# Optimization experiments

Measured on AMD Instinct MI355X. Metric: run time of the kernel, lower is better.

Reference implementation:

```python
import jax, jax.numpy as jnp
import numpy as np

TILE = 128

def _dequant(Wq, scales, zeros):
    # Wq: [out, n_cols] int codes; scales/zeros: [n_tiles, out]
    n_cols = Wq.shape[1]
    tids = jnp.arange(n_cols) // TILE            # tile id per column
    s = scales[tids].T                           # [out, n_cols]
    z = zeros[tids].T                            # [out, n_cols]
    return (Wq.astype(jnp.float32) - z) * s

def setup_inputs() -> dict:
    key = jax.random.key(0)
    ks = jax.random.split(key, 9)
    B, IN, OUT = 256, 8192, 8192
    n_high, n_low = 2048, 6144
    nt_hi, nt_lo = 16, 48
    x = jax.random.normal(ks[0], (B, IN), dtype=jnp.float32)
    W_high_q = jax.random.randint(ks[1], (OUT, n_high), 0, 64, dtype=jnp.int32)
    W_low_q = jax.random.randint(ks[2], (OUT, n_low), 0, 32, dtype=jnp.int32)
    scales_high = jax.random.uniform(ks[3], (nt_hi, OUT), dtype=jnp.float32, minval=0.001, maxval=0.05)
    zeros_high = jax.random.normal(ks[4], (nt_hi, OUT), dtype=jnp.float32) * 16.0
    scales_low = jax.random.uniform(ks[5], (nt_lo, OUT), dtype=jnp.float32, minval=0.001, maxval=0.05)
    zeros_low = jax.random.normal(ks[6], (nt_lo, OUT), dtype=jnp.float32) * 8.0
    bias = jax.random.normal(ks[7], (OUT,), dtype=jnp.float32) * 0.02
    col_indices = jax.random.permutation(ks[8], IN).astype(jnp.int32)
    return {"x": x, "W_high_q": W_high_q, "W_low_q": W_low_q,
            "scales_high": scales_high, "zeros_high": zeros_high,
            "scales_low": scales_low, "zeros_low": zeros_low,
            "bias": bias, "col_indices": col_indices}

def reference(x, W_high_q, W_low_q, scales_high, zeros_high,
              scales_low, zeros_low, bias, col_indices):
    # Dequantize both precision regions (per-tile affine: (q - zero) * scale)
    W_high = _dequant(W_high_q, scales_high, zeros_high)   # [out, n_high]
    W_low = _dequant(W_low_q, scales_low, zeros_low)       # [out, n_low]
    W_perm = jnp.concatenate([W_high, W_low], axis=1)      # [out, in]
    # y = x @ W.T where W[:, col_indices] = W_perm  <=>  gather x columns instead
    x_perm = x[:, col_indices]                             # [B, in]
    return x_perm @ W_perm.T + bias[None, :]
```

## Files before the change

### kernel.cpp

```cpp
#include <hip/hip_runtime.h>
#include <stdint.h>


#define IN_DIM 8192
#define OUT_DIM 8192
#define BDIM 256
#define NH 2048
#define NL 6144
#define BN 64
#define BK 32
#define KSPLIT 4
#define KSEG (IN_DIM / KSPLIT)
#define NSTEP (KSEG / BK)

typedef __bf16 bf16x8 __attribute__((ext_vector_type(8)));
typedef float f32x4 __attribute__((ext_vector_type(4)));

__device__ __forceinline__ unsigned short bfbits(float f) {
  union { float f; unsigned int u; } v; v.f = f;
  unsigned int u = v.u;
  u += 0x7fffu + ((u >> 16) & 1u);
  return (unsigned short)(u >> 16);
}
__device__ __forceinline__ unsigned int pk2(float a, float b) {
  return (unsigned int)bfbits(a) | ((unsigned int)bfbits(b) << 16);
}

extern "C" __global__ void gather_k(const float* __restrict__ x,
                                    const int* __restrict__ ci,
                                    unsigned short* __restrict__ xp) {
  int i4 = blockIdx.x * blockDim.x + threadIdx.x;
  int b = i4 >> 11;
  int k4 = (i4 & 2047) << 2;
  int4 c = *(const int4*)(ci + k4);
  const float* xr = x + (size_t)b * IN_DIM;
  uint2 st;
  st.x = pk2(xr[c.x], xr[c.y]);
  st.y = pk2(xr[c.z], xr[c.w]);
  *(uint2*)(xp + (size_t)b * IN_DIM + k4) = st;
}

extern "C" __global__ __launch_bounds__(256, 2)
void gemm_k(const unsigned short* __restrict__ xp,
            const int* __restrict__ Whq, const int* __restrict__ Wlq,
            const float* __restrict__ sh, const float* __restrict__ zh,
            const float* __restrict__ sl, const float* __restrict__ zl,
            const float* __restrict__ bias,
            float* __restrict__ outp,
            int use_atomic)
{
  __shared__ char smem[2 * 16384 + 2 * 4096];
  const int t = threadIdx.x;
  const int lane = t & 63;
  const int wv = t >> 6;
  const int nblk = blockIdx.x;
  const int kh = blockIdx.y;
  const int n0 = nblk * BN;
  const int l15 = lane & 15;
  const int g4 = lane >> 4;

  const int xr = t >> 2;
  const int xc = (t & 3) ^ (xr & 3);
  const unsigned short* xg0 = xp + (size_t)xr * IN_DIM + (size_t)kh * KSEG + xc * 8;

  const int wcol = t >> 2;
  const int wm = t & 3;
  const int oo = n0 + wcol;
  const int* wb0 = (kh == 0) ? (Whq + (size_t)oo * NH)
                             : (Wlq + (size_t)oo * NL + (size_t)(kh - 1) * KSEG);
  const float* sb = (kh == 0) ? (sh + oo) : (sl + (size_t)(kh - 1) * 16 * OUT_DIM + oo);
  const float* zb = (kh == 0) ? (zh + oo) : (zl + (size_t)(kh - 1) * 16 * OUT_DIM + oo);

  f32x4 acc[4][4];
  {
    float bvj[4];
    #pragma unroll
    for (int j = 0; j < 4; ++j)
      bvj[j] = (kh == 0) ? bias[n0 + j * 16 + l15] : 0.f;
    #pragma unroll
    for (int i = 0; i < 4; ++i)
      #pragma unroll
      for (int j = 0; j < 4; ++j) {
        acc[i][j][0] = bvj[j]; acc[i][j][1] = bvj[j];
        acc[i][j][2] = bvj[j]; acc[i][j][3] = bvj[j];
      }
  }

  int4 q0, q1; float sc, zs;

  auto stage_x = [&](int bx, int s) {
    const unsigned short* g = xg0 + s * BK;
    char* lb = smem + bx * 16384 + wv * 1024;
    #pragma unroll
    for (int r = 0; r < 4; ++r)
      __builtin_amdgcn_global_load_lds(
          (const __attribute__((address_space(1))) void*)(g + (size_t)r * 64 * IN_DIM),
          (__attribute__((address_space(3))) void*)(lb + r * 4096), 16, 0, 0);
  };
  auto stage_w_load = [&](int s) {
    const int* p = wb0 + s * BK + wm * 8;
    q0 = *(const int4*)p;
    q1 = *(const int4*)(p + 4);
    float s_ = sb[(s >> 2) * OUT_DIM];
    float z_ = zb[(s >> 2) * OUT_DIM];
    sc = s_; zs = z_ * s_;
  };
  auto stage_w_write = [&](int bx) {
    uint4 d;
    d.x = pk2((float)q0.x * sc - zs, (float)q0.y * sc - zs);
    d.y = pk2((float)q0.z * sc - zs, (float)q0.w * sc - zs);
    d.z = pk2((float)q1.x * sc - zs, (float)q1.y * sc - zs);
    d.w = pk2((float)q1.z * sc - zs, (float)q1.w * sc - zs);
    char* wb = smem + 32768 + bx * 4096;
    *(uint4*)(wb + wcol * 64 + ((wm ^ (wcol & 3)) * 16)) = d;
  };
  auto compute = [&](int bx) {
    const char* xb = smem + bx * 16384;
    const char* wbuf = smem + 32768 + bx * 4096;
    bf16x8 a[4], b[4];
    #pragma unroll
    for (int i = 0; i < 4; ++i) {
      int row = wv * 64 + i * 16 + l15;
      int ch = g4 ^ (row & 3);
      a[i] = *(const bf16x8*)(xb + row * 64 + ch * 16);
    }
    #pragma unroll
    for (int j = 0; j < 4; ++j) {
      int col = j * 16 + l15;
      int ch = g4 ^ (col & 3);
      b[j] = *(const bf16x8*)(wbuf + col * 64 + ch * 16);
    }
    #pragma unroll
    for (int i = 0; i < 4; ++i)
      #pragma unroll
      for (int j = 0; j < 4; ++j)
        acc[i][j] = __builtin_amdgcn_mfma_f32_16x16x32_bf16(a[i], b[j], acc[i][j], 0, 0, 0);
  };

  stage_x(0, 0);
  stage_w_load(0);
  stage_w_write(0);
  __syncthreads();

  #pragma unroll 1
  for (int s = 0; s < NSTEP; s += 2) {
    stage_x(1, s + 1);
    stage_w_load(s + 1);
    compute(0);
    stage_w_write(1);
    __syncthreads();
    if (s + 2 < NSTEP) { stage_x(0, s + 2); stage_w_load(s + 2); }
    compute(1);
    if (s + 2 < NSTEP) stage_w_write(0);
    __syncthreads();
  }

  if (use_atomic) {
    #pragma unroll
    for (int i = 0; i < 4; ++i) {
      int row0 = wv * 64 + i * 16 + g4 * 4;
      #pragma unroll
      for (int j = 0; j < 4; ++j) {
        int col = n0 + j * 16 + l15;
        #pragma unroll
        for (int r = 0; r < 4; ++r)
          atomicAdd(&outp[(size_t)(row0 + r) * OUT_DIM + col], acc[i][j][r]);
      }
    }
  } else {
    float* pp = outp + (size_t)kh * ((size_t)BDIM * OUT_DIM);
    #pragma unroll
    for (int i = 0; i < 4; ++i) {
      int row0 = wv * 64 + i * 16 + g4 * 4;
      #pragma unroll
      for (int j = 0; j < 4; ++j) {
        int col = n0 + j * 16 + l15;
        #pragma unroll
        for (int r = 0; r < 4; ++r)
          pp[(size_t)(row0 + r) * OUT_DIM + col] = acc[i][j][r];
      }
    }
  }
}

extern "C" __global__ void reduce_k(const float* __restrict__ part,
                                    float* __restrict__ out) {
  int i4 = blockIdx.x * blockDim.x + threadIdx.x;
  size_t off = (size_t)i4 * 4;
  const size_t S = (size_t)BDIM * OUT_DIM;
  float4 p0 = *(const float4*)(part + off);
  float4 p1 = *(const float4*)(part + off + S);
  float4 p2 = *(const float4*)(part + off + 2 * S);
  float4 p3 = *(const float4*)(part + off + 3 * S);
  float4 r;
  r.x = p0.x + p1.x + p2.x + p3.x;
  r.y = p0.y + p1.y + p2.y + p3.y;
  r.z = p0.z + p1.z + p2.z + p3.z;
  r.w = p0.w + p1.w + p2.w + p3.w;
  *(float4*)(out + off) = r;
}

extern "C" void kernel_launch(void* const* d_in, const int* in_sizes, int n_in,
                              void* d_out, int out_size, void* d_ws, size_t ws_size,
                              hipStream_t stream) {
  const float* x   = (const float*)d_in[0];
  const int* Whq   = (const int*)d_in[1];
  const int* Wlq   = (const int*)d_in[2];
  const float* sh  = (const float*)d_in[3];
  const float* zh  = (const float*)d_in[4];
  const float* sl  = (const float*)d_in[5];
  const float* zl  = (const float*)d_in[6];
  const float* bias = (const float*)d_in[7];
  const int* ci    = (const int*)d_in[8];
  float* out = (float*)d_out;

  unsigned short* xp = (unsigned short*)d_ws;
  const size_t XP_BYTES = (size_t)BDIM * IN_DIM * 2;
  const size_t PART_BYTES = (size_t)KSPLIT * BDIM * OUT_DIM * 4;
  bool have_ws = ws_size >= XP_BYTES + PART_BYTES;

  gather_k<<<dim3(2048), dim3(256), 0, stream>>>(x, ci, xp);

  dim3 gg(OUT_DIM / BN, KSPLIT);
  if (have_ws) {
    float* part = (float*)((char*)d_ws + XP_BYTES);
    gemm_k<<<gg, dim3(256), 0, stream>>>(xp, Whq, Wlq, sh, zh, sl, zl, bias, part, 0);
    reduce_k<<<dim3(2048), dim3(256), 0, stream>>>(part, out);
  } else {
    hipMemsetAsync(d_out, 0, (size_t)out_size * sizeof(float), stream);
    gemm_k<<<gg, dim3(256), 0, stream>>>(xp, Whq, Wlq, sh, zh, sl, zl, bias, out, 1);
  }
}
```

Measured before the change: 398.6 us.

## Prefetch quantized weights two steps ahead and stage scales in LDS

Preloads all per-tile scales and scale*zero products for the block into shared memory once, instead of fetching them from global memory each step. Weight codes are now loaded two K-steps ahead into double register sets, so global latency has more compute to hide behind. The loop is peeled and uses hand-placed waitcnt, s_barrier and sched_barrier in place of __syncthreads, which allows partial vmcnt waits. This raises register pressure and makes correctness depend on the exact waitcnt counts.

```diff
diff --git a/kernel.cpp b/kernel.cpp
--- a/kernel.cpp
+++ b/kernel.cpp
@@ -12,6 +12,12 @@
 #define KSPLIT 4
 #define KSEG (IN_DIM / KSPLIT)
 #define NSTEP (KSEG / BK)
+#define NTILE (KSEG / 128)
+
+#define XOFF 0
+#define WOFF 32768
+#define SCOFF 40960
+#define ZSOFF 45056
 
 typedef __bf16 bf16x8 __attribute__((ext_vector_type(8)));
 typedef float f32x4 __attribute__((ext_vector_type(4)));
@@ -49,13 +55,12 @@
             float* __restrict__ outp,
             int use_atomic)
 {
-  __shared__ char smem[2 * 16384 + 2 * 4096];
+  __shared__ char smem[49152];
   const int t = threadIdx.x;
   const int lane = t & 63;
   const int wv = t >> 6;
-  const int nblk = blockIdx.x;
   const int kh = blockIdx.y;
-  const int n0 = nblk * BN;
+  const int n0 = blockIdx.x * BN;
   const int l15 = lane & 15;
   const int g4 = lane >> 4;
 
@@ -65,11 +70,10 @@
 
   const int wcol = t >> 2;
   const int wm = t & 3;
-  const int oo = n0 + wcol;
-  const int* wb0 = (kh == 0) ? (Whq + (size_t)oo * NH)
-                             : (Wlq + (size_t)oo * NL + (size_t)(kh - 1) * KSEG);
-  const float* sb = (kh == 0) ? (sh + oo) : (sl + (size_t)(kh - 1) * 16 * OUT_DIM + oo);
-  const float* zb = (kh == 0) ? (zh + oo) : (zl + (size_t)(kh - 1) * 16 * OUT_DIM + oo);
+  const int* wb0 = (kh == 0) ? (Whq + (size_t)(n0 + wcol) * NH)
+                             : (Wlq + (size_t)(n0 + wcol) * NL + (size_t)(kh - 1) * KSEG);
+  const float* sbase = ((kh == 0) ? sh : sl + (size_t)(kh - 1) * NTILE * OUT_DIM) + n0;
+  const float* zbase = ((kh == 0) ? zh : zl + (size_t)(kh - 1) * NTILE * OUT_DIM) + n0;
 
   f32x4 acc[4][4];
   {
@@ -86,37 +90,34 @@
       }
   }
 
-  int4 q0, q1; float sc, zs;
-
   auto stage_x = [&](int bx, int s) {
     const unsigned short* g = xg0 + s * BK;
-    char* lb = smem + bx * 16384 + wv * 1024;
+    char* lb = smem + XOFF + bx * 16384 + wv * 1024;
     #pragma unroll
     for (int r = 0; r < 4; ++r)
       __builtin_amdgcn_global_load_lds(
           (const __attribute__((address_space(1))) void*)(g + (size_t)r * 64 * IN_DIM),
           (__attribute__((address_space(3))) void*)(lb + r * 4096), 16, 0, 0);
   };
-  auto stage_w_load = [&](int s) {
+  auto wload = [&](int4& a, int4& b, int s) {
     const int* p = wb0 + s * BK + wm * 8;
-    q0 = *(const int4*)p;
-    q1 = *(const int4*)(p + 4);
-    float s_ = sb[(s >> 2) * OUT_DIM];
-    float z_ = zb[(s >> 2) * OUT_DIM];
-    sc = s_; zs = z_ * s_;
-  };
-  auto stage_w_write = [&](int bx) {
+    a = *(const int4*)p;
+    b = *(const int4*)(p + 4);
+  };
+  auto wdeq = [&](int bx, int4 a, int4 b, int s) {
+    int tl = s >> 2;
+    float sc = *(const float*)(smem + SCOFF + (tl * 64 + wcol) * 4);
+    float zs = *(const float*)(smem + ZSOFF + (tl * 64 + wcol) * 4);
     uint4 d;
-    d.x = pk2((float)q0.x * sc - zs, (float)q0.y * sc - zs);
-    d.y = pk2((float)q0.z * sc - zs, (float)q0.w * sc - zs);
-    d.z = pk2((float)q1.x * sc - zs, (float)q1.y * sc - zs);
-    d.w = pk2((float)q1.z * sc - zs, (float)q1.w * sc - zs);
-    char* wb = smem + 32768 + bx * 4096;
-    *(uint4*)(wb + wcol * 64 + ((wm ^ (wcol & 3)) * 16)) = d;
+    d.x = pk2((float)a.x * sc - zs, (float)a.y * sc - zs);
+    d.y = pk2((float)a.z * sc - zs, (float)a.w * sc - zs);
+    d.z = pk2((float)b.x * sc - zs, (float)b.y * sc - zs);
+    d.w = pk2((float)b.z * sc - zs, (float)b.w * sc - zs);
+    *(uint4*)(smem + WOFF + bx * 4096 + wcol * 64 + ((wm ^ (wcol & 3)) * 16)) = d;
   };
   auto compute = [&](int bx) {
-    const char* xb = smem + bx * 16384;
-    const char* wbuf = smem + 32768 + bx * 4096;
+    const char* xb = smem + XOFF + bx * 16384;
+    const char* wbuf = smem + WOFF + bx * 4096;
     bf16x8 a[4], b[4];
     #pragma unroll
     for (int i = 0; i < 4; ++i) {
@@ -137,23 +138,53 @@
         acc[i][j] = __builtin_amdgcn_mfma_f32_16x16x32_bf16(a[i], b[j], acc[i][j], 0, 0, 0);
   };
 
+  #pragma unroll
+  for (int r = 0; r < 4; ++r) {
+    int p = t + r * 256;
+    float s_ = sbase[(size_t)(p >> 6) * OUT_DIM + (p & 63)];
+    float z_ = zbase[(size_t)(p >> 6) * OUT_DIM + (p & 63)];
+    *(float*)(smem + SCOFF + p * 4) = s_;
+    *(float*)(smem + ZSOFF + p * 4) = z_ * s_;
+  }
   stage_x(0, 0);
-  stage_w_load(0);
-  stage_w_write(0);
+  int4 qa0, qa1, qb0, qb1;
+  wload(qa0, qa1, 0);
+  wload(qb0, qb1, 1);
   __syncthreads();
+  wdeq(0, qa0, qa1, 0);
+  asm volatile("s_waitcnt lgkmcnt(0)" ::: "memory");
+  __builtin_amdgcn_s_barrier();
 
   #pragma unroll 1
-  for (int s = 0; s < NSTEP; s += 2) {
+  for (int it = 0; it < 31; ++it) {
+    const int s = it * 2;
+    __builtin_amdgcn_sched_barrier(0);
     stage_x(1, s + 1);
-    stage_w_load(s + 1);
+    __builtin_amdgcn_sched_barrier(0);
+    wload(qa0, qa1, s + 2);
+    __builtin_amdgcn_sched_barrier(0);
     compute(0);
-    stage_w_write(1);
-    __syncthreads();
-    if (s + 2 < NSTEP) { stage_x(0, s + 2); stage_w_load(s + 2); }
+    wdeq(1, qb0, qb1, s + 1);
+    asm volatile("s_waitcnt vmcnt(2) lgkmcnt(0)" ::: "memory");
+    __builtin_amdgcn_s_barrier();
+    __builtin_amdgcn_sched_barrier(0);
+    stage_x(0, s + 2);
+    __builtin_amdgcn_sched_barrier(0);
+    wload(qb0, qb1, s + 3);
+    __builtin_amdgcn_sched_barrier(0);
     compute(1);
-    if (s + 2 < NSTEP) stage_w_write(0);
-    __syncthreads();
-  }
+    wdeq(0, qa0, qa1, s + 2);
+    asm volatile("s_waitcnt vmcnt(2) lgkmcnt(0)" ::: "memory");
+    __builtin_amdgcn_s_barrier();
+  }
+  __builtin_amdgcn_sched_barrier(0);
+  stage_x(1, 63);
+  __builtin_amdgcn_sched_barrier(0);
+  compute(0);
+  wdeq(1, qb0, qb1, 63);
+  asm volatile("s_waitcnt vmcnt(0) lgkmcnt(0)" ::: "memory");
+  __builtin_amdgcn_s_barrier();
+  compute(1);
 
   if (use_atomic) {
     #pragma unroll
```

Measured after the change: 388.1 us. -2.6%, faster.

## Widen GEMM tiles, stream int weights to LDS, dequantize in registers

Applied to the files above, without the earlier changes.

Each block now owns 256 output columns over a 1024-wide K segment, with 512 threads and an 8-way K split that maps onto a single 1-D grid. This cuts redundant re-reads of the activation tile across column blocks. Raw int32 weight codes are copied straight into a triple-buffered LDS area with global_load_lds, and per-tile scales and zero·scale products are preloaded into LDS. Dequantization to bf16 happens in registers right before each MFMA, and sched_barrier, setprio and manual vmcnt waits interleave loads with compute. In exchange it uses a large LDS footprint (one block per CU) and writes a larger partial-sum buffer, which the templated reduce kernel then has to read back.

```diff
diff --git a/kernel.cpp b/kernel.cpp
--- a/kernel.cpp
+++ b/kernel.cpp
@@ -7,11 +7,17 @@
 #define BDIM 256
 #define NH 2048
 #define NL 6144
-#define BN 64
+#define BN 256
 #define BK 32
-#define KSPLIT 4
-#define KSEG (IN_DIM / KSPLIT)
-#define NSTEP (KSEG / BK)
+#define KSPLIT 8
+#define KSEG 1024
+#define NTIL 32
+#define NT 8
+
+#define XOFF 0
+#define WOFF 32768
+#define SCOFF 131072
+#define ZSOFF 139264
 
 typedef __bf16 bf16x8 __attribute__((ext_vector_type(8)));
 typedef float f32x4 __attribute__((ext_vector_type(4)));
@@ -26,9 +32,9 @@
   return (unsigned int)bfbits(a) | ((unsigned int)bfbits(b) << 16);
 }
 
-extern "C" __global__ void gather_k(const float* __restrict__ x,
-                                    const int* __restrict__ ci,
-                                    unsigned short* __restrict__ xp) {
+__global__ void gather_k(const float* __restrict__ x,
+                         const int* __restrict__ ci,
+                         unsigned short* __restrict__ xp) {
   int i4 = blockIdx.x * blockDim.x + threadIdx.x;
   int b = i4 >> 11;
   int k4 = (i4 & 2047) << 2;
@@ -40,7 +46,96 @@
   *(uint2*)(xp + (size_t)b * IN_DIM + k4) = st;
 }
 
-extern "C" __global__ __launch_bounds__(256, 2)
+#define PH_OPEN \
+  __builtin_amdgcn_sched_barrier(0); \
+  __builtin_amdgcn_s_barrier(); \
+  __builtin_amdgcn_sched_barrier(0)
+
+#define STAGE_X(S) { \
+  _Pragma("unroll") \
+  for (int q_ = 0; q_ < 2; ++q_) \
+    __builtin_amdgcn_global_load_lds( \
+      (const __attribute__((address_space(1))) void*)(xsrc + (size_t)q_ * 128 * IN_DIM * 2 + (S) * 64), \
+      (__attribute__((address_space(3))) void*)(smem + XOFF + ((S) & 1) * 16384 + q_ * 8192 + wv * 1024), \
+      16, 0, 0); \
+}
+
+#define STAGE_WQ(S, BUF, Q) \
+  __builtin_amdgcn_global_load_lds( \
+    (const __attribute__((address_space(1))) void*)(wsrc + (size_t)(Q) * 64 * ldw + (S) * 32), \
+    (__attribute__((address_space(3))) void*)(smem + WOFF + (BUF) * 32768 + (Q) * 8192 + wv * 1024), \
+    16, 0, 0);
+
+#define BREAD(WBP, J, U0, U1) { \
+  int col_ = wc64 + (J) * 16 + l15; \
+  const char* bp_ = (WBP) + col_ * 128; \
+  U0 = *(const int4*)(bp_ + (((2 * g4) ^ (col_ & 7)) * 16)); \
+  U1 = *(const int4*)(bp_ + (((2 * g4 + 1) ^ (col_ & 7)) * 16)); \
+}
+
+#define MFMA8(BJ, J) { \
+  _Pragma("unroll") \
+  for (int i_ = 0; i_ < 8; ++i_) \
+    acc[i_][J] = __builtin_amdgcn_mfma_f32_16x16x32_bf16(aF[i_], BJ, acc[i_][J], 0, 0, 0); \
+}
+
+#define TILE(T, ISSX, ISSW, VMST) { \
+  const int xb_ = (T) & 1, wb_ = (T) % 3, wb2_ = ((T) + 2) % 3; \
+  const char* xbp_ = smem + XOFF + xb_ * 16384; \
+  const char* wbp_ = smem + WOFF + wb_ * 32768; \
+  const int tl_ = (T) >> 2; \
+   \
+  bf16x8 aF[8]; \
+  _Pragma("unroll") \
+  for (int i_ = 0; i_ < 8; ++i_) { \
+    int row_ = wr128 + i_ * 16 + l15; \
+    aF[i_] = *(const bf16x8*)(xbp_ + row_ * 64 + ((g4 ^ (row_ & 3)) * 16)); \
+  } \
+  float scf_[4], zsf_[4]; \
+  _Pragma("unroll") \
+  for (int j_ = 0; j_ < 4; ++j_) { \
+    int sidx_ = (tl_ * 256 + wc64 + j_ * 16 + l15) * 4; \
+    scf_[j_] = *(const float*)(smem + SCOFF + sidx_); \
+    zsf_[j_] = *(const float*)(smem + ZSOFF + sidx_); \
+  } \
+  int4 u0_, u1_; \
+  BREAD(wbp_, 0, u0_, u1_); \
+  if (ISSX) STAGE_X((T) + 1); \
+  PH_OPEN; \
+  __builtin_amdgcn_s_setprio(1); \
+  { bf16x8 b_ = dq8(u0_, u1_, scf_[0], zsf_[0]); MFMA8(b_, 0); } \
+  __builtin_amdgcn_s_setprio(0); \
+  PH_OPEN; \
+   \
+  BREAD(wbp_, 1, u0_, u1_); \
+  if (ISSW) { STAGE_WQ((T) + 2, wb2_, 0); STAGE_WQ((T) + 2, wb2_, 1); } \
+  PH_OPEN; \
+  __builtin_amdgcn_s_setprio(1); \
+  { bf16x8 b_ = dq8(u0_, u1_, scf_[1], zsf_[1]); MFMA8(b_, 1); } \
+  __builtin_amdgcn_s_setprio(0); \
+  PH_OPEN; \
+   \
+  BREAD(wbp_, 2, u0_, u1_); \
+  if (ISSW) { STAGE_WQ((T) + 2, wb2_, 2); STAGE_WQ((T) + 2, wb2_, 3); } \
+  PH_OPEN; \
+  __builtin_amdgcn_s_setprio(1); \
+  { bf16x8 b_ = dq8(u0_, u1_, scf_[2], zsf_[2]); MFMA8(b_, 2); } \
+  __builtin_amdgcn_s_setprio(0); \
+  PH_OPEN; \
+   \
+  BREAD(wbp_, 3, u0_, u1_); \
+  PH_OPEN; \
+  __builtin_amdgcn_s_setprio(1); \
+  { bf16x8 b_ = dq8(u0_, u1_, scf_[3], zsf_[3]); MFMA8(b_, 3); } \
+  __builtin_amdgcn_s_setprio(0); \
+  __builtin_amdgcn_sched_barrier(0); \
+  VMST; \
+  __builtin_amdgcn_sched_barrier(0); \
+  __builtin_amdgcn_s_barrier(); \
+  __builtin_amdgcn_sched_barrier(0); \
+}
+
+__global__ __launch_bounds__(512, 1)
 void gemm_k(const unsigned short* __restrict__ xp,
             const int* __restrict__ Whq, const int* __restrict__ Wlq,
             const float* __restrict__ sh, const float* __restrict__ zh,
@@ -49,119 +144,81 @@
             float* __restrict__ outp,
             int use_atomic)
 {
-  __shared__ char smem[2 * 16384 + 2 * 4096];
+  __shared__ __attribute__((aligned(16))) char smem[147456];
   const int t = threadIdx.x;
   const int lane = t & 63;
   const int wv = t >> 6;
-  const int nblk = blockIdx.x;
-  const int kh = blockIdx.y;
-  const int n0 = nblk * BN;
+  const int wr128 = (wv >> 2) * 128;
+  const int wc64 = (wv & 3) * 64;
   const int l15 = lane & 15;
   const int g4 = lane >> 4;
 
-  const int xr = t >> 2;
-  const int xc = (t & 3) ^ (xr & 3);
-  const unsigned short* xg0 = xp + (size_t)xr * IN_DIM + (size_t)kh * KSEG + xc * 8;
-
-  const int wcol = t >> 2;
-  const int wm = t & 3;
-  const int oo = n0 + wcol;
-  const int* wb0 = (kh == 0) ? (Whq + (size_t)oo * NH)
-                             : (Wlq + (size_t)oo * NL + (size_t)(kh - 1) * KSEG);
-  const float* sb = (kh == 0) ? (sh + oo) : (sl + (size_t)(kh - 1) * 16 * OUT_DIM + oo);
-  const float* zb = (kh == 0) ? (zh + oo) : (zl + (size_t)(kh - 1) * 16 * OUT_DIM + oo);
-
-  f32x4 acc[4][4];
-  {
-    float bvj[4];
+  const int kh = blockIdx.x & 7;
+  const int n0 = (blockIdx.x >> 3) * BN;
+  const bool hi = (kh < 2);
+
+  const char* xsrc = (const char*)xp + (size_t)(t >> 2) * (IN_DIM * 2)
+                   + (size_t)kh * KSEG * 2 + (((t & 3) ^ ((t >> 2) & 3)) * 16);
+  const int wcol0 = t >> 3;
+  const int ldw = hi ? NH : NL;
+  const int* wsrc = (hi ? Whq + (size_t)kh * KSEG : Wlq + (size_t)(kh - 2) * KSEG)
+                  + (size_t)(n0 + wcol0) * ldw + ((t & 7) ^ (wcol0 & 7)) * 4;
+
+  const float* sbase = (hi ? sh + (size_t)kh * NT * OUT_DIM
+                           : sl + (size_t)(kh - 2) * NT * OUT_DIM) + n0;
+  const float* zbase = (hi ? zh + (size_t)kh * NT * OUT_DIM
+                           : zl + (size_t)(kh - 2) * NT * OUT_DIM) + n0;
+
+  auto dq8 = [&](int4 a, int4 b, float sc, float zs) -> bf16x8 {
+    bf16x8 r;
+    r[0] = (__bf16)((float)a.x * sc - zs);
+    r[1] = (__bf16)((float)a.y * sc - zs);
+    r[2] = (__bf16)((float)a.z * sc - zs);
+    r[3] = (__bf16)((float)a.w * sc - zs);
+    r[4] = (__bf16)((float)b.x * sc - zs);
+    r[5] = (__bf16)((float)b.y * sc - zs);
+    r[6] = (__bf16)((float)b.z * sc - zs);
+    r[7] = (__bf16)((float)b.w * sc - zs);
+    return r;
+  };
+
+  f32x4 acc[8][4];
+  #pragma unroll
+  for (int j = 0; j < 4; ++j) {
+    float bv = (kh == 0) ? bias[n0 + wc64 + j * 16 + l15] : 0.f;
     #pragma unroll
-    for (int j = 0; j < 4; ++j)
-      bvj[j] = (kh == 0) ? bias[n0 + j * 16 + l15] : 0.f;
+    for (int i = 0; i < 8; ++i) {
+      acc[i][j][0] = bv; acc[i][j][1] = bv; acc[i][j][2] = bv; acc[i][j][3] = bv;
+    }
+  }
+
+  #pragma unroll
+  for (int r = 0; r < 4; ++r) {
+    int p = t + r * 512;
+    float s_ = sbase[(size_t)(p >> 8) * OUT_DIM + (p & 255)];
+    float z_ = zbase[(size_t)(p >> 8) * OUT_DIM + (p & 255)];
+    *(float*)(smem + SCOFF + p * 4) = s_;
+    *(float*)(smem + ZSOFF + p * 4) = z_ * s_;
+  }
+  STAGE_X(0);
+  STAGE_WQ(0, 0, 0); STAGE_WQ(0, 0, 1); STAGE_WQ(0, 0, 2); STAGE_WQ(0, 0, 3);
+  STAGE_WQ(1, 1, 0); STAGE_WQ(1, 1, 1); STAGE_WQ(1, 1, 2); STAGE_WQ(1, 1, 3);
+  __syncthreads();
+
+  #pragma unroll 1
+  for (int tt = 0; tt < 30; ++tt) {
+    TILE(tt, true, true, asm volatile("s_waitcnt vmcnt(4)"));
+  }
+  TILE(30, true, false, asm volatile("s_waitcnt vmcnt(0)"));
+  TILE(31, false, false, (void)0);
+
+  if (use_atomic) {
     #pragma unroll
-    for (int i = 0; i < 4; ++i)
+    for (int i = 0; i < 8; ++i) {
+      int row0 = wr128 + i * 16 + g4 * 4;
       #pragma unroll
       for (int j = 0; j < 4; ++j) {
-        acc[i][j][0] = bvj[j]; acc[i][j][1] = bvj[j];
-        acc[i][j][2] = bvj[j]; acc[i][j][3] = bvj[j];
-      }
-  }
-
-  int4 q0, q1; float sc, zs;
-
-  auto stage_x = [&](int bx, int s) {
-    const unsigned short* g = xg0 + s * BK;
-    char* lb = smem + bx * 16384 + wv * 1024;
-    #pragma unroll
-    for (int r = 0; r < 4; ++r)
-      __builtin_amdgcn_global_load_lds(
-          (const __attribute__((address_space(1))) void*)(g + (size_t)r * 64 * IN_DIM),
-          (__attribute__((address_space(3))) void*)(lb + r * 4096), 16, 0, 0);
-  };
-  auto stage_w_load = [&](int s) {
-    const int* p = wb0 + s * BK + wm * 8;
-    q0 = *(const int4*)p;
-    q1 = *(const int4*)(p + 4);
-    float s_ = sb[(s >> 2) * OUT_DIM];
-    float z_ = zb[(s >> 2) * OUT_DIM];
-    sc = s_; zs = z_ * s_;
-  };
-  auto stage_w_write = [&](int bx) {
-    uint4 d;
-    d.x = pk2((float)q0.x * sc - zs, (float)q0.y * sc - zs);
-    d.y = pk2((float)q0.z * sc - zs, (float)q0.w * sc - zs);
-    d.z = pk2((float)q1.x * sc - zs, (float)q1.y * sc - zs);
-    d.w = pk2((float)q1.z * sc - zs, (float)q1.w * sc - zs);
-    char* wb = smem + 32768 + bx * 4096;
-    *(uint4*)(wb + wcol * 64 + ((wm ^ (wcol & 3)) * 16)) = d;
-  };
-  auto compute = [&](int bx) {
-    const char* xb = smem + bx * 16384;
-    const char* wbuf = smem + 32768 + bx * 4096;
-    bf16x8 a[4], b[4];
-    #pragma unroll
-    for (int i = 0; i < 4; ++i) {
-      int row = wv * 64 + i * 16 + l15;
-      int ch = g4 ^ (row & 3);
-      a[i] = *(const bf16x8*)(xb + row * 64 + ch * 16);
-    }
-    #pragma unroll
-    for (int j = 0; j < 4; ++j) {
-      int col = j * 16 + l15;
-      int ch = g4 ^ (col & 3);
-      b[j] = *(const bf16x8*)(wbuf + col * 64 + ch * 16);
-    }
-    #pragma unroll
-    for (int i = 0; i < 4; ++i)
-      #pragma unroll
-      for (int j = 0; j < 4; ++j)
-        acc[i][j] = __builtin_amdgcn_mfma_f32_16x16x32_bf16(a[i], b[j], acc[i][j], 0, 0, 0);
-  };
-
-  stage_x(0, 0);
-  stage_w_load(0);
-  stage_w_write(0);
-  __syncthreads();
-
-  #pragma unroll 1
-  for (int s = 0; s < NSTEP; s += 2) {
-    stage_x(1, s + 1);
-    stage_w_load(s + 1);
-    compute(0);
-    stage_w_write(1);
-    __syncthreads();
-    if (s + 2 < NSTEP) { stage_x(0, s + 2); stage_w_load(s + 2); }
-    compute(1);
-    if (s + 2 < NSTEP) stage_w_write(0);
-    __syncthreads();
-  }
-
-  if (use_atomic) {
-    #pragma unroll
-    for (int i = 0; i < 4; ++i) {
-      int row0 = wv * 64 + i * 16 + g4 * 4;
-      #pragma unroll
-      for (int j = 0; j < 4; ++j) {
-        int col = n0 + j * 16 + l15;
+        int col = n0 + wc64 + j * 16 + l15;
         #pragma unroll
         for (int r = 0; r < 4; ++r)
           atomicAdd(&outp[(size_t)(row0 + r) * OUT_DIM + col], acc[i][j][r]);
@@ -170,11 +227,11 @@
   } else {
     float* pp = outp + (size_t)kh * ((size_t)BDIM * OUT_DIM);
     #pragma unroll
-    for (int i = 0; i < 4; ++i) {
-      int row0 = wv * 64 + i * 16 + g4 * 4;
+    for (int i = 0; i < 8; ++i) {
+      int row0 = wr128 + i * 16 + g4 * 4;
       #pragma unroll
       for (int j = 0; j < 4; ++j) {
-        int col = n0 + j * 16 + l15;
+        int col = n0 + wc64 + j * 16 + l15;
         #pragma unroll
         for (int r = 0; r < 4; ++r)
           pp[(size_t)(row0 + r) * OUT_DIM + col] = acc[i][j][r];
@@ -183,20 +240,18 @@
   }
 }
 
-extern "C" __global__ void reduce_k(const float* __restrict__ part,
-                                    float* __restrict__ out) {
+template<int NS>
+__global__ void reduce_k(const float* __restrict__ part,
+                         float* __restrict__ out) {
   int i4 = blockIdx.x * blockDim.x + threadIdx.x;
   size_t off = (size_t)i4 * 4;
   const size_t S = (size_t)BDIM * OUT_DIM;
-  float4 p0 = *(const float4*)(part + off);
-  float4 p1 = *(const float4*)(part + off + S);
-  float4 p2 = *(const float4*)(part + off + 2 * S);
-  float4 p3 = *(const float4*)(part + off + 3 * S);
-  float4 r;
-  r.x = p0.x + p1.x + p2.x + p3.x;
-  r.y = p0.y + p1.y + p2.y + p3.y;
-  r.z = p0.z + p1.z + p2.z + p3.z;
-  r.w = p0.w + p1.w + p2.w + p3.w;
+  float4 r = *(const float4*)(part + off);
+  #pragma unroll
+  for (int k = 1; k < NS; ++k) {
+    float4 p = *(const float4*)(part + off + (size_t)k * S);
+    r.x += p.x; r.y += p.y; r.z += p.z; r.w += p.w;
+  }
   *(float4*)(out + off) = r;
 }
 
@@ -221,13 +276,13 @@
 
   gather_k<<<dim3(2048), dim3(256), 0, stream>>>(x, ci, xp);
 
-  dim3 gg(OUT_DIM / BN, KSPLIT);
+  dim3 gg(KSPLIT * (OUT_DIM / BN));
   if (have_ws) {
     float* part = (float*)((char*)d_ws + XP_BYTES);
-    gemm_k<<<gg, dim3(256), 0, stream>>>(xp, Whq, Wlq, sh, zh, sl, zl, bias, part, 0);
-    reduce_k<<<dim3(2048), dim3(256), 0, stream>>>(part, out);
+    gemm_k<<<gg, dim3(512), 0, stream>>>(xp, Whq, Wlq, sh, zh, sl, zl, bias, part, 0);
+    reduce_k<KSPLIT><<<dim3(2048), dim3(256), 0, stream>>>(part, out);
   } else {
     hipMemsetAsync(d_out, 0, (size_t)out_size * sizeof(float), stream);
-    gemm_k<<<gg, dim3(256), 0, stream>>>(xp, Whq, Wlq, sh, zh, sl, zl, bias, out, 1);
-  }
-}
+    gemm_k<<<gg, dim3(512), 0, stream>>>(xp, Whq, Wlq, sh, zh, sl, zl, bias, out, 1);
+  }
+}
```

Measured after the change: 400.5 us. About the same (+0.5%).
